# Performance work log

Measured on AMD Instinct MI355X. Metric: run time of the kernel, lower is better.

Reference implementation:

```python
import jax, jax.numpy as jnp
import numpy as np

G = 5      # kan_grid: number of grid intervals on [-1, 1]
K = 3      # kan_k: B-spline order

def make_grid(in_dim, dtype=jnp.float32):
    # pykan extended grid: uniform on [-1,1] with G intervals, extended by K knots each side
    h = 2.0 / G
    pts = jnp.arange(-K, G + K + 1, dtype=dtype) * h - 1.0   # (G + 2K + 1,)
    return jnp.broadcast_to(pts, (in_dim, G + 2 * K + 1))

def b_spline_basis(x, grid):
    # x: (N, D), grid: (D, M).  Cox-de Boor recursion, vectorized over (N, D).
    xe = x[:, :, None]                      # (N, D, 1)
    g = grid[None, :, :]                    # (1, D, M)
    B = ((xe >= g[:, :, :-1]) & (xe < g[:, :, 1:])).astype(x.dtype)  # order 0
    for p in range(1, K + 1):
        B = ((xe - g[:, :, :-(p + 1)]) / (g[:, :, p:-1] - g[:, :, :-(p + 1)])) * B[:, :, :-1] \
          + ((g[:, :, p + 1:] - xe) / (g[:, :, p + 1:] - g[:, :, 1:-p])) * B[:, :, 1:]
    return B                                # (N, D, G + K)

def kan_layer(x, coef, scale_base, scale_sp):
    # pykan KANLayer: out_o = sum_i [ sb[i,o]*silu(x_i) + ss[i,o]*sum_g B(x_i)_g * coef[i,o,g] ]
    in_dim = x.shape[1]
    B = b_spline_basis(x, make_grid(in_dim, x.dtype))          # (N, D, G+K)
    y_base = jnp.einsum('ni,io->no', jax.nn.silu(x), scale_base)
    y_sp = jnp.einsum('nig,iog,io->no', B, coef, scale_sp)
    return y_base + y_sp

def setup_inputs() -> dict:
    key = jax.random.key(0)
    ks = jax.random.split(key, 5)
    d_model, hidden = 512, 1024
    bsz, seq = 4, 1024
    ncoef = G + K
    x = jax.random.normal(ks[0], (bsz, seq, d_model), dtype=jnp.float32)
    coef1 = 0.1 * jax.random.normal(ks[1], (d_model, hidden, ncoef), dtype=jnp.float32)
    coef2 = 0.1 * jax.random.normal(ks[2], (hidden, d_model, ncoef), dtype=jnp.float32)
    scale_base1 = (1.0 / np.sqrt(d_model)) * jax.random.normal(ks[3], (d_model, hidden), dtype=jnp.float32)
    scale_base2 = (1.0 / np.sqrt(hidden)) * jax.random.normal(ks[4], (hidden, d_model), dtype=jnp.float32)
    scale_sp1 = jnp.ones((d_model, hidden), dtype=jnp.float32)
    scale_sp2 = jnp.ones((hidden, d_model), dtype=jnp.float32)
    return {"x": x, "coef1": coef1, "scale_base1": scale_base1, "scale_sp1": scale_sp1,
            "coef2": coef2, "scale_base2": scale_base2, "scale_sp2": scale_sp2}

def reference(x, coef1, scale_base1, scale_sp1, coef2, scale_base2, scale_sp2):
    bsz, seq, d_model = x.shape
    flat = x.reshape(-1, d_model)                      # (N, d_model); chunking is math-neutral
    h = kan_layer(flat, coef1, scale_base1, scale_sp1)  # (N, hidden)
    out = kan_layer(h, coef2, scale_base2, scale_sp2)   # (N, d_model)
    return out.reshape(bsz, seq, d_model)              # dropout p=0.0 -> identity
```

## Files before the change

### kernel.cpp

```cpp
#include <hip/hip_runtime.h>
#include <hip/hip_bf16.h>
#include <cstdint>
#include <cstddef>

typedef float  f32x4 __attribute__((ext_vector_type(4)));
typedef _Float16 f16x8 __attribute__((ext_vector_type(8)));

#define DEVFN __device__ __forceinline__

DEVFN void bspline8(float x, float bv[8]) {
    float t[12];
#pragma unroll
    for (int j = 0; j < 12; ++j) t[j] = (float)(j - 3) * 0.4f - 1.0f;
    float B[11];
#pragma unroll
    for (int j = 0; j < 11; ++j) B[j] = (x >= t[j] && x < t[j + 1]) ? 1.0f : 0.0f;
    const float rp[3] = {2.5f, 1.25f, 0.8333333333f};
#pragma unroll
    for (int p = 1; p <= 3; ++p) {
#pragma unroll
        for (int j = 0; j + p < 11; ++j) {
            float left  = (x - t[j]) * rp[p - 1];
            float right = (t[j + p + 1] - x) * rp[p - 1];
            B[j] = left * B[j] + right * B[j + 1];
        }
    }
#pragma unroll
    for (int g = 0; g < 8; ++g) bv[g] = B[g];
}

__global__ void prep_a_kernel(const float* __restrict__ X,
                              _Float16* __restrict__ Aaug,
                              int total, int dshift) {
    int idx = blockIdx.x * 256 + threadIdx.x;
    if (idx >= total) return;
    const int D = 1 << dshift;
    const int K = 9 << dshift;
    const int n = idx >> dshift;
    const int i = idx & (D - 1);
    float x = X[idx];
    float s = x * __builtin_amdgcn_rcpf(1.0f + __expf(-x));
    float bv[8];
    bspline8(x, bv);
    _Float16* dst = Aaug + (size_t)n * K + i;
    dst[0] = (_Float16)s;
#pragma unroll
    for (int g = 0; g < 8; ++g) dst[(size_t)(g + 1) * D] = (_Float16)bv[g];
}

__global__ void prep_w_kernel(const float* __restrict__ coef,
                              const float* __restrict__ sb,
                              const float* __restrict__ sp,
                              _Float16* __restrict__ WT,
                              int total, int din_shift, int dout) {
    int idx = blockIdx.x * 256 + threadIdx.x;
    if (idx >= total) return;
    const int Din = 1 << din_shift;
    const int i = idx & (Din - 1);
    const int o = idx >> din_shift;
    const size_t K = (size_t)9 << din_shift;
    const size_t cidx = (size_t)i * dout + o;
    float base  = sb[cidx];
    float scale = sp[cidx];
    const float* cp = coef + cidx * 8;
    _Float16* dst = WT + (size_t)o * K + i;
    dst[0] = (_Float16)base;
#pragma unroll
    for (int g = 0; g < 8; ++g) dst[(size_t)(g + 1) * Din] = (_Float16)(cp[g] * scale);
}

DEVFN void gload16(const void* g, void* l) {
    __builtin_amdgcn_global_load_lds(
        (const __attribute__((address_space(1))) void*)g,
        (__attribute__((address_space(3))) void*)l, 16, 0, 0);
}

__global__ __launch_bounds__(256) void gemm128_f16_bt(
    const _Float16* __restrict__ A,
    const _Float16* __restrict__ WT,
    float* __restrict__ C,
    int K, int N, int klen, int gxshift) {
    constexpr int BK = 64;
    __shared__ _Float16 Alds[2][128 * BK];
    __shared__ _Float16 Blds[2][128 * BK];

    const int tid  = threadIdx.x;
    const int lane = tid & 63;
    const int w    = tid >> 6;
    const int wm   = w >> 1;
    const int wn   = w & 1;

    const int gx   = 1 << gxshift;
    const int nwg  = gx * 32 * gridDim.z;
    const int orig = blockIdx.x + (blockIdx.y << gxshift) + blockIdx.z * (gx * 32);
    const int tile = (orig & 7) * (nwg >> 3) + (orig >> 3);
    const int col  = tile & (gx - 1);
    const int rs   = tile >> gxshift;
    const int row  = rs & 31;
    const int spl  = rs >> 5;

    const size_t bm = (size_t)row * 128;
    const size_t bn = (size_t)col * 128;
    const int kbase = spl * klen;
    const int nt    = klen / BK;

    const f32x4 vzero = {0.0f, 0.0f, 0.0f, 0.0f};
    f32x4 acc[4][4];
#pragma unroll
    for (int m = 0; m < 4; ++m)
#pragma unroll
        for (int n = 0; n < 4; ++n) acc[m][n] = vzero;

    const int srow = tid >> 3;
    const int c8   = tid & 7;
    const int ldst = w * 512;

#define STAGE(b, kk)                                                         \
    {                                                                        \
        _Pragma("unroll")                                                    \
        for (int is = 0; is < 4; ++is) {                                     \
            const int r  = is * 32 + srow;                                   \
            const int sg = (c8 ^ (r & 7)) << 3;                              \
            gload16(A + (bm + r) * (size_t)K + (kk) + sg,                    \
                    &Alds[b][is * 2048 + ldst]);                             \
            gload16(WT + (bn + r) * (size_t)K + (kk) + sg,                   \
                    &Blds[b][is * 2048 + ldst]);                             \
        }                                                                    \
    }

    STAGE(0, kbase);

    for (int t = 0; t < nt; ++t) {
        const int cur = t & 1;
        if (t + 1 < nt) {
            STAGE(cur ^ 1, kbase + (t + 1) * BK);
            asm volatile("s_waitcnt vmcnt(8)" ::: "memory");
        } else {
            asm volatile("s_waitcnt vmcnt(0)" ::: "memory");
        }
        __builtin_amdgcn_s_barrier();
        __builtin_amdgcn_sched_barrier(0);

#pragma unroll
        for (int ks = 0; ks < BK; ks += 32) {
            f16x8 af[4], bf[4];
            const int g = (ks >> 3) + (lane >> 4);
#pragma unroll
            for (int m = 0; m < 4; ++m) {
                const int r2 = wm * 64 + m * 16 + (lane & 15);
                af[m] = *(const f16x8*)(&Alds[cur][r2 * BK + ((g ^ (r2 & 7)) << 3)]);
            }
#pragma unroll
            for (int n = 0; n < 4; ++n) {
                const int r2 = wn * 64 + n * 16 + (lane & 15);
                bf[n] = *(const f16x8*)(&Blds[cur][r2 * BK + ((g ^ (r2 & 7)) << 3)]);
            }
#pragma unroll
            for (int m = 0; m < 4; ++m)
#pragma unroll
                for (int n = 0; n < 4; ++n)
                    acc[m][n] = __builtin_amdgcn_mfma_f32_16x16x32_f16(
                        af[m], bf[n], acc[m][n], 0, 0, 0);
        }
        __builtin_amdgcn_s_barrier();
        __builtin_amdgcn_sched_barrier(0);
    }
#undef STAGE

    const int r0 = wm * 64 + (lane >> 4) * 4;
    const int c0 = wn * 64 + (lane & 15);
#pragma unroll
    for (int m = 0; m < 4; ++m)
#pragma unroll
        for (int n = 0; n < 4; ++n)
#pragma unroll
            for (int r = 0; r < 4; ++r)
                unsafeAtomicAdd(&C[(bm + r0 + m * 16 + r) * (size_t)N + bn + c0 + n * 16],
                                acc[m][n][r]);
}

extern "C" void kernel_launch(void* const* d_in, const int* in_sizes, int n_in,
                              void* d_out, int out_size, void* d_ws, size_t ws_size,
                              hipStream_t stream) {
    const float* x     = (const float*)d_in[0];
    const float* coef1 = (const float*)d_in[1];
    const float* sb1   = (const float*)d_in[2];
    const float* sp1   = (const float*)d_in[3];
    const float* coef2 = (const float*)d_in[4];
    const float* sb2   = (const float*)d_in[5];
    const float* sp2   = (const float*)d_in[6];
    float* out = (float*)d_out;

    const int M  = 4096;
    const int D1 = 512;
    const int D2 = 1024;
    const int K1 = 9 * D1;
    const int K2 = 9 * D2;

    char* ws = (char*)d_ws;
    float*    h    = (float*)ws;
    _Float16* Aaug = (_Float16*)(ws + (size_t)M * D2 * 4);
    _Float16* WT   = (_Float16*)(ws + (size_t)M * D2 * 4 + (size_t)M * K2 * 2);

    hipMemsetAsync(h, 0, (size_t)M * D2 * 4, stream);
    hipMemsetAsync(out, 0, (size_t)M * D1 * 4, stream);

    prep_w_kernel<<<(D1 * D2) / 256, 256, 0, stream>>>(coef1, sb1, sp1, WT,
                                                       D1 * D2, 9, D2);
    prep_a_kernel<<<(M * D1) / 256, 256, 0, stream>>>(x, Aaug, M * D1, 9);
    {
        dim3 grid(D2 / 128, M / 128, 2);
        gemm128_f16_bt<<<grid, 256, 0, stream>>>(Aaug, WT, h, K1, D2, K1 / 2, 3);
    }
    prep_w_kernel<<<(D2 * D1) / 256, 256, 0, stream>>>(coef2, sb2, sp2, WT,
                                                       D1 * D2, 10, D1);
    prep_a_kernel<<<(M * D2) / 256, 256, 0, stream>>>(h, Aaug, M * D2, 10);
    {
        dim3 grid(D1 / 128, M / 128, 4);
        gemm128_f16_bt<<<grid, 256, 0, stream>>>(Aaug, WT, out, K2, D1, K2 / 4, 2);
    }
}
```

Baseline: 279.1 us.

## Use 256x256 GEMM tiles with split-K partial buffers instead of atomics

The GEMM tile grows from 128x128 (256 threads) to 256x256 (512 threads), which raises data reuse per LDS load. Split-K results are now written as plain stores into separate partial buffers rather than accumulated with float atomics. The partials are summed by the next layer's feature-prep kernel, and by a new reduce kernel for the final output, which also removes the memsets. The cost is more register and LDS pressure, 128 KB of LDS per block, and extra partial-buffer memory traffic.

```diff
diff --git a/kernel.cpp b/kernel.cpp
--- a/kernel.cpp
+++ b/kernel.cpp
@@ -27,6 +27,15 @@
     }
 #pragma unroll
     for (int g = 0; g < 8; ++g) bv[g] = B[g];
+}
+
+DEVFN void kan_features(float x, _Float16* dst, int D) {
+    float s = x * __builtin_amdgcn_rcpf(1.0f + __expf(-x));
+    float bv[8];
+    bspline8(x, bv);
+    dst[0] = (_Float16)s;
+#pragma unroll
+    for (int g = 0; g < 8; ++g) dst[(size_t)(g + 1) * D] = (_Float16)bv[g];
 }
 
 __global__ void prep_a_kernel(const float* __restrict__ X,
@@ -38,14 +47,33 @@
     const int K = 9 << dshift;
     const int n = idx >> dshift;
     const int i = idx & (D - 1);
-    float x = X[idx];
-    float s = x * __builtin_amdgcn_rcpf(1.0f + __expf(-x));
-    float bv[8];
-    bspline8(x, bv);
-    _Float16* dst = Aaug + (size_t)n * K + i;
-    dst[0] = (_Float16)s;
-#pragma unroll
-    for (int g = 0; g < 8; ++g) dst[(size_t)(g + 1) * D] = (_Float16)bv[g];
+    kan_features(X[idx], Aaug + (size_t)n * K + i, D);
+}
+
+__global__ void prep_a_red_kernel(const float* __restrict__ HP,
+                                  _Float16* __restrict__ Aaug,
+                                  int total, int dshift, size_t pstride) {
+    int idx = blockIdx.x * 256 + threadIdx.x;
+    if (idx >= total) return;
+    const int D = 1 << dshift;
+    const int K = 9 << dshift;
+    const int n = idx >> dshift;
+    const int i = idx & (D - 1);
+    float x = (HP[idx] + HP[idx + pstride]) +
+              (HP[idx + 2 * pstride] + HP[idx + 3 * pstride]);
+    kan_features(x, Aaug + (size_t)n * K + i, D);
+}
+
+__global__ void reduce_out_kernel(const float* __restrict__ OP,
+                                  float* __restrict__ out,
+                                  int total4, size_t pstride4) {
+    int i = blockIdx.x * 256 + threadIdx.x;
+    if (i >= total4) return;
+    const f32x4* p = (const f32x4*)OP;
+    f32x4 s = p[i];
+#pragma unroll
+    for (int k = 1; k < 8; ++k) s += p[i + k * pstride4];
+    ((f32x4*)out)[i] = s;
 }
 
 __global__ void prep_w_kernel(const float* __restrict__ coef,
@@ -75,39 +103,40 @@
         (__attribute__((address_space(3))) void*)l, 16, 0, 0);
 }
 
-__global__ __launch_bounds__(256) void gemm128_f16_bt(
+__global__ __launch_bounds__(512, 2) void gemm256_f16_bt(
     const _Float16* __restrict__ A,
     const _Float16* __restrict__ WT,
-    float* __restrict__ C,
+    float* __restrict__ P,
     int K, int N, int klen, int gxshift) {
     constexpr int BK = 64;
-    __shared__ _Float16 Alds[2][128 * BK];
-    __shared__ _Float16 Blds[2][128 * BK];
+    __shared__ _Float16 Alds[2][256 * BK];
+    __shared__ _Float16 Blds[2][256 * BK];
 
     const int tid  = threadIdx.x;
     const int lane = tid & 63;
     const int w    = tid >> 6;
-    const int wm   = w >> 1;
-    const int wn   = w & 1;
+    const int wm   = w >> 2;
+    const int wn   = w & 3;
 
     const int gx   = 1 << gxshift;
-    const int nwg  = gx * 32 * gridDim.z;
-    const int orig = blockIdx.x + (blockIdx.y << gxshift) + blockIdx.z * (gx * 32);
+    const int nwg  = gx * 16 * gridDim.z;
+    const int orig = blockIdx.x + (blockIdx.y << gxshift) + blockIdx.z * (gx * 16);
     const int tile = (orig & 7) * (nwg >> 3) + (orig >> 3);
     const int col  = tile & (gx - 1);
     const int rs   = tile >> gxshift;
-    const int row  = rs & 31;
-    const int spl  = rs >> 5;
-
-    const size_t bm = (size_t)row * 128;
-    const size_t bn = (size_t)col * 128;
+    const int row  = rs & 15;
+    const int spl  = rs >> 4;
+
+    const size_t bm = (size_t)row * 256;
+    const size_t bn = (size_t)col * 256;
     const int kbase = spl * klen;
     const int nt    = klen / BK;
+    float* Cp = P + (size_t)spl * 4096 * N;
 
     const f32x4 vzero = {0.0f, 0.0f, 0.0f, 0.0f};
-    f32x4 acc[4][4];
-#pragma unroll
-    for (int m = 0; m < 4; ++m)
+    f32x4 acc[8][4];
+#pragma unroll
+    for (int m = 0; m < 8; ++m)
 #pragma unroll
         for (int n = 0; n < 4; ++n) acc[m][n] = vzero;
 
@@ -119,12 +148,12 @@
     {                                                                        \
         _Pragma("unroll")                                                    \
         for (int is = 0; is < 4; ++is) {                                     \
-            const int r  = is * 32 + srow;                                   \
+            const int r  = is * 64 + srow;                                   \
             const int sg = (c8 ^ (r & 7)) << 3;                              \
             gload16(A + (bm + r) * (size_t)K + (kk) + sg,                    \
-                    &Alds[b][is * 2048 + ldst]);                             \
+                    &Alds[b][is * 4096 + ldst]);                             \
             gload16(WT + (bn + r) * (size_t)K + (kk) + sg,                   \
-                    &Blds[b][is * 2048 + ldst]);                             \
+                    &Blds[b][is * 4096 + ldst]);                             \
         }                                                                    \
     }
 
@@ -143,11 +172,11 @@
 
 #pragma unroll
         for (int ks = 0; ks < BK; ks += 32) {
-            f16x8 af[4], bf[4];
+            f16x8 af[8], bf[4];
             const int g = (ks >> 3) + (lane >> 4);
 #pragma unroll
-            for (int m = 0; m < 4; ++m) {
-                const int r2 = wm * 64 + m * 16 + (lane & 15);
+            for (int m = 0; m < 8; ++m) {
+                const int r2 = wm * 128 + m * 16 + (lane & 15);
                 af[m] = *(const f16x8*)(&Alds[cur][r2 * BK + ((g ^ (r2 & 7)) << 3)]);
             }
 #pragma unroll
@@ -156,7 +185,7 @@
                 bf[n] = *(const f16x8*)(&Blds[cur][r2 * BK + ((g ^ (r2 & 7)) << 3)]);
             }
 #pragma unroll
-            for (int m = 0; m < 4; ++m)
+            for (int m = 0; m < 8; ++m)
 #pragma unroll
                 for (int n = 0; n < 4; ++n)
                     acc[m][n] = __builtin_amdgcn_mfma_f32_16x16x32_f16(
@@ -167,16 +196,16 @@
     }
 #undef STAGE
 
-    const int r0 = wm * 64 + (lane >> 4) * 4;
+    const int r0 = wm * 128 + (lane >> 4) * 4;
     const int c0 = wn * 64 + (lane & 15);
 #pragma unroll
-    for (int m = 0; m < 4; ++m)
+    for (int m = 0; m < 8; ++m)
 #pragma unroll
         for (int n = 0; n < 4; ++n)
 #pragma unroll
             for (int r = 0; r < 4; ++r)
-                unsafeAtomicAdd(&C[(bm + r0 + m * 16 + r) * (size_t)N + bn + c0 + n * 16],
-                                acc[m][n][r]);
+                Cp[(bm + r0 + m * 16 + r) * (size_t)N + bn + c0 + n * 16] =
+                    acc[m][n][r];
 }
 
 extern "C" void kernel_launch(void* const* d_in, const int* in_sizes, int n_in,
@@ -198,25 +227,26 @@
     const int K2 = 9 * D2;
 
     char* ws = (char*)d_ws;
-    float*    h    = (float*)ws;
-    _Float16* Aaug = (_Float16*)(ws + (size_t)M * D2 * 4);
-    _Float16* WT   = (_Float16*)(ws + (size_t)M * D2 * 4 + (size_t)M * K2 * 2);
-
-    hipMemsetAsync(h, 0, (size_t)M * D2 * 4, stream);
-    hipMemsetAsync(out, 0, (size_t)M * D1 * 4, stream);
+    _Float16* Aaug = (_Float16*)ws;
+    _Float16* WT   = (_Float16*)(ws + (size_t)M * K2 * 2);
+    float*    P    = (float*)(ws + (size_t)M * K2 * 2 +
+                              (size_t)D1 * K2 * 2);
 
     prep_w_kernel<<<(D1 * D2) / 256, 256, 0, stream>>>(coef1, sb1, sp1, WT,
                                                        D1 * D2, 9, D2);
     prep_a_kernel<<<(M * D1) / 256, 256, 0, stream>>>(x, Aaug, M * D1, 9);
     {
-        dim3 grid(D2 / 128, M / 128, 2);
-        gemm128_f16_bt<<<grid, 256, 0, stream>>>(Aaug, WT, h, K1, D2, K1 / 2, 3);
+        dim3 grid(D2 / 256, M / 256, 4);
+        gemm256_f16_bt<<<grid, 512, 0, stream>>>(Aaug, WT, P, K1, D2, K1 / 4, 2);
     }
     prep_w_kernel<<<(D2 * D1) / 256, 256, 0, stream>>>(coef2, sb2, sp2, WT,
                                                        D1 * D2, 10, D1);
-    prep_a_kernel<<<(M * D2) / 256, 256, 0, stream>>>(h, Aaug, M * D2, 10);
+    prep_a_red_kernel<<<(M * D2) / 256, 256, 0, stream>>>(P, Aaug, M * D2, 10,
+                                                          (size_t)M * D2);
     {
-        dim3 grid(D1 / 128, M / 128, 4);
-        gemm128_f16_bt<<<grid, 256, 0, stream>>>(Aaug, WT, out, K2, D1, K2 / 4, 2);
-    }
-}
+        dim3 grid(D1 / 256, M / 256, 8);
+        gemm256_f16_bt<<<grid, 512, 0, stream>>>(Aaug, WT, P, K2, D1, K2 / 8, 1);
+    }
+    reduce_out_kernel<<<(M * D1 / 4) / 256, 256, 0, stream>>>(
+        P, out, M * D1 / 4, (size_t)M * D1 / 4);
+}
```

Measured after the change: 252.6 us. 1.1x faster.
